# Kernel optimization log

Hardware: AMD Instinct MI355X
Metric: run time of the kernel (lower is better)

Reference implementation:

```python
import jax, jax.numpy as jnp
import numpy as np

V, D, H, DH, DI, L = 10000, 512, 8, 64, 2048, 12
B, S = 4, 1024
MAX_KLEN = 1024 + 0 + 512  # tgt_len + ext_len + mem_len
EPS = 1e-5
STD = 0.02


def setup_inputs() -> dict:
    key = jax.random.key(0)
    ks = jax.random.split(key, 10)
    data = jax.random.randint(ks[0], (B, S), 0, V)
    word_emb = jax.random.normal(ks[1], (V, D), jnp.float32) * STD
    pos_emb = jax.random.normal(ks[2], (MAX_KLEN, D), jnp.float32) * STD
    Wq = jax.random.normal(ks[3], (L, H * DH, D), jnp.float32) * STD
    Wkv = jax.random.normal(ks[4], (L, 2 * H * DH, D), jnp.float32) * STD
    Wo = jax.random.normal(ks[5], (L, D, H * DH), jnp.float32) * STD
    ln1_g = jnp.ones((L, D), jnp.float32)
    ln1_b = jnp.zeros((L, D), jnp.float32)
    W1 = jax.random.normal(ks[6], (L, DI, D), jnp.float32) * STD
    b1 = jnp.zeros((L, DI), jnp.float32)
    W2 = jax.random.normal(ks[7], (L, D, DI), jnp.float32) * STD
    b2 = jnp.zeros((L, D), jnp.float32)
    ln2_g = jnp.ones((L, D), jnp.float32)
    ln2_b = jnp.zeros((L, D), jnp.float32)
    out_b = jnp.zeros((V,), jnp.float32)  # out_layer weight is tied to word_emb
    return dict(data=data, word_emb=word_emb, pos_emb=pos_emb, Wq=Wq, Wkv=Wkv,
                Wo=Wo, ln1_g=ln1_g, ln1_b=ln1_b, W1=W1, b1=b1, W2=W2, b2=b2,
                ln2_g=ln2_g, ln2_b=ln2_b, out_b=out_b)


def _layernorm(x, g, b):
    m = jnp.mean(x, axis=-1, keepdims=True)
    v = jnp.mean((x - m) ** 2, axis=-1, keepdims=True)
    return (x - m) * jax.lax.rsqrt(v + EPS) * g + b


def reference(data, word_emb, pos_emb, Wq, Wkv, Wo, ln1_g, ln1_b,
              W1, b1, W2, b2, ln2_g, ln2_b, out_b):
    # mems start empty -> mlen = 0, klen = qlen, standard causal mask.
    h = word_emb[data] + pos_emb[:S][None, :, :]      # [B, S, D]
    mask = jnp.triu(jnp.ones((S, S), bool), 1)        # True above diagonal
    scale = 1.0 / np.sqrt(DH)

    def layer(h, p):
        wq, wkv, wo, g1, bl1, w1, bf1, w2, bf2, g2, bl2 = p
        q = (h @ wq.T).reshape(B, S, H, DH)
        k, v = jnp.split(h @ wkv.T, 2, axis=-1)
        k = k.reshape(B, S, H, DH)
        v = v.reshape(B, S, H, DH)
        sc = jnp.einsum('bqhd,bkhd->bhqk', q, k) * scale
        sc = jnp.where(mask[None, None], -jnp.inf, sc)
        p_attn = jax.nn.softmax(sc, axis=-1)           # [B, H, S, S] materialized
        av = jnp.einsum('bhqk,bkhd->bqhd', p_attn, v).reshape(B, S, H * DH)
        h = _layernorm(h + av @ wo.T, g1, bl1)         # post-LN (pre_lnorm=False)
        ff = jax.nn.relu(h @ w1.T + bf1) @ w2.T + bf2
        h = _layernorm(h + ff, g2, bl2)
        return h, None

    h, _ = jax.lax.scan(layer, h,
                        (Wq, Wkv, Wo, ln1_g, ln1_b, W1, b1, W2, b2, ln2_g, ln2_b))
    logits = h @ word_emb.T + out_b                    # tied output projection
    return logits                                      # [B, S, V]
```

## Files before the change

### kernel.cpp

```cpp
#include <hip/hip_runtime.h>

#define VV 10000
#define DD 512
#define HH 8
#define DH 64
#define DI 2048
#define LL 12
#define BB 4
#define SS 1024
#define TT (BB * SS)


typedef __attribute__((ext_vector_type(8))) short bhalf8;
typedef __attribute__((ext_vector_type(16))) float f32x16;

__device__ __forceinline__ void split_bf16(float x, unsigned short& h, unsigned short& l)
{
    unsigned int u = __float_as_uint(x);
    unsigned int r = (u + 0x7FFFu + ((u >> 16) & 1u)) & 0xFFFF0000u;
    h = (unsigned short)(r >> 16);
    float lf = x - __uint_as_float(r);
    unsigned int ul = __float_as_uint(lf);
    l = (unsigned short)((ul + 0x7FFFu + ((ul >> 16) & 1u)) >> 16);
}

__global__ __launch_bounds__(256) void convsplit(
    const float* __restrict__ src, unsigned short* __restrict__ hi,
    unsigned short* __restrict__ lo, int n4)
{
    int stride = gridDim.x * 256;
    for (int i = blockIdx.x * 256 + threadIdx.x; i < n4; i += stride) {
        float4 v = ((const float4*)src)[i];
        ushort4 h, l;
        split_bf16(v.x, h.x, l.x);
        split_bf16(v.y, h.y, l.y);
        split_bf16(v.z, h.z, l.z);
        split_bf16(v.w, h.w, l.w);
        ((ushort4*)hi)[i] = h;
        ((ushort4*)lo)[i] = l;
    }
}

__global__ __launch_bounds__(256) void embed_kernel(
    const int* __restrict__ data, const float* __restrict__ we,
    const float* __restrict__ pe, float* __restrict__ h,
    unsigned short* __restrict__ hhi, unsigned short* __restrict__ hlo)
{
    int tok = blockIdx.x;
    int tid = threadIdx.x;
    int idx = data[tok];
    int s = tok & (SS - 1);
    size_t base = (size_t)tok * DD;
    size_t wb = (size_t)idx * DD;
    size_t pb = (size_t)s * DD;
    float a = we[wb + tid] + pe[pb + tid];
    float b = we[wb + 256 + tid] + pe[pb + 256 + tid];
    h[base + tid] = a;
    h[base + 256 + tid] = b;
    unsigned short hx, lx;
    split_bf16(a, hx, lx); hhi[base + tid] = hx;       hlo[base + tid] = lx;
    split_bf16(b, hx, lx); hhi[base + 256 + tid] = hx; hlo[base + 256 + tid] = lx;
}

template<int BN, int EPI, bool SWZ>
__global__ __launch_bounds__(256) void gemm_mfma(
    const unsigned short* __restrict__ Ahp, const unsigned short* __restrict__ Alp,
    const unsigned short* __restrict__ Whp, const unsigned short* __restrict__ Wlp,
    const float* __restrict__ bias, float* __restrict__ C,
    unsigned short* __restrict__ Chp, unsigned short* __restrict__ Clp,
    unsigned short* __restrict__ Vhp, unsigned short* __restrict__ Vlp,
    int N, int K)
{
    constexpr int FN  = BN / 64;
    constexpr int BT  = BN * 128;
    constexpr int NBG = BN / 8;
    constexpr int NGRP = 32 + 2 * NBG;
    constexpr int PW  = NGRP / 4;
    __shared__ __align__(16) char smem[32768 + 2 * BT];

    int bx = blockIdx.x, by = blockIdx.y;
    if (SWZ) {
        int nwg = gridDim.x * gridDim.y;
        int id = by * gridDim.x + bx;
        int nq = nwg >> 3, rr = nwg & 7;
        int xcd = id & 7, j = id >> 3;
        int nid = (xcd < rr) ? (xcd * (nq + 1) + j)
                             : (rr * (nq + 1) + (xcd - rr) * nq + j);
        bx = nid % gridDim.x;
        by = nid / gridDim.x;
    }

    const int tid   = threadIdx.x;
    const int lane  = tid & 63;
    const int wid   = tid >> 6;
    const int wm    = wid >> 1;
    const int wn    = wid & 1;
    const int laneM = lane & 31;
    const int laneK = lane >> 5;
    const int m0    = by * 128;
    const int n0    = bx * BN;
    const int srow8 = lane >> 3;
    const int sslot = lane & 7;

    f32x16 acc[2][FN];
    #pragma unroll
    for (int i = 0; i < 2; ++i)
        #pragma unroll
        for (int j = 0; j < FN; ++j)
            #pragma unroll
            for (int r = 0; r < 16; ++r) acc[i][j][r] = 0.f;

    for (int k0 = 0; k0 < K; k0 += 64) {
        __syncthreads();
        bhalf8 rbuf[PW];
        #pragma unroll
        for (int t = 0; t < PW; ++t) {
            int g = wid * PW + t;
            const unsigned short* src;
            if (g < 32) {
                const unsigned short* bp = (g < 16) ? Ahp : Alp;
                int row = (g & 15) * 8 + srow8;
                src = bp + (size_t)(m0 + row) * K + (k0 + sslot * 8);
            } else {
                int d = g - 32;
                const unsigned short* bp = (d < NBG) ? Whp : Wlp;
                int row = (d & (NBG - 1)) * 8 + srow8;
                int n = n0 + row;
                n = (n < N) ? n : (N - 1);
                src = bp + (size_t)n * K + (k0 + sslot * 8);
            }
            rbuf[t] = *(const bhalf8*)src;
        }
        #pragma unroll
        for (int t = 0; t < PW; ++t) {
            int g = wid * PW + t;
            int off;
            if (g < 32) {
                int row = (g & 15) * 8 + srow8;
                off = ((g >> 4) << 14) + sslot * 2048 + ((row ^ sslot) << 4);
            } else {
                int d = g - 32;
                int row = (d & (NBG - 1)) * 8 + srow8;
                off = 32768 + ((d < NBG) ? 0 : BT)
                    + sslot * (BN * 16) + ((row ^ sslot) << 4);
            }
            *(bhalf8*)(smem + off) = rbuf[t];
        }
        __syncthreads();

        #pragma unroll
        for (int kb = 0; kb < 4; ++kb) {
            const int slot = kb * 2 + laneK;
            bhalf8 ah[2], al[2], bh[FN], bl[FN];
            #pragma unroll
            for (int i = 0; i < 2; ++i) {
                int row = wm * 64 + i * 32 + laneM;
                int off = slot * 2048 + ((row ^ slot) << 4);
                ah[i] = *(const bhalf8*)(smem + off);
                al[i] = *(const bhalf8*)(smem + 16384 + off);
            }
            #pragma unroll
            for (int j = 0; j < FN; ++j) {
                int row = wn * (BN / 2) + j * 32 + laneM;
                int off = 32768 + slot * (BN * 16) + ((row ^ slot) << 4);
                bh[j] = *(const bhalf8*)(smem + off);
                bl[j] = *(const bhalf8*)(smem + BT + off);
            }
            #pragma unroll
            for (int i = 0; i < 2; ++i)
                #pragma unroll
                for (int j = 0; j < FN; ++j) {
                    acc[i][j] = __builtin_amdgcn_mfma_f32_32x32x16_bf16(ah[i], bh[j], acc[i][j], 0, 0, 0);
                    acc[i][j] = __builtin_amdgcn_mfma_f32_32x32x16_bf16(ah[i], bl[j], acc[i][j], 0, 0, 0);
                    acc[i][j] = __builtin_amdgcn_mfma_f32_32x32x16_bf16(al[i], bh[j], acc[i][j], 0, 0, 0);
                }
        }
    }

    #pragma unroll
    for (int j = 0; j < FN; ++j) {
        int ncol = n0 + wn * (BN / 2) + j * 32 + laneM;
        bool nok = (ncol < N);
        float bv = 0.f;
        if (EPI == 1 || EPI == 2) { if (nok) bv = bias[ncol]; }
        #pragma unroll
        for (int i = 0; i < 2; ++i) {
            #pragma unroll
            for (int r = 0; r < 16; ++r) {
                int mrow = m0 + wm * 64 + i * 32 + (r & 3) + ((r >> 2) << 3) + laneK * 4;
                float v = acc[i][j][r] + bv;
                if (EPI == 2) v = fmaxf(v, 0.f);
                if (nok) {
                    if (EPI == 2 || EPI == 3) {
                        unsigned short hx, lx;
                        split_bf16(v, hx, lx);
                        Chp[(size_t)mrow * N + ncol] = hx;
                        Clp[(size_t)mrow * N + ncol] = lx;
                    } else if (EPI == 4) {
                        unsigned short hx, lx;
                        split_bf16(v, hx, lx);
                        if (ncol < 512) {
                            Chp[(size_t)mrow * 512 + ncol] = hx;
                            Clp[(size_t)mrow * 512 + ncol] = lx;
                        } else {
                            Vhp[(size_t)(ncol - 512) * TT + mrow] = hx;
                            Vlp[(size_t)(ncol - 512) * TT + mrow] = lx;
                        }
                    } else {
                        C[(size_t)mrow * N + ncol] = v;
                    }
                }
            }
        }
    }
}

__global__ __launch_bounds__(128) void flash_mfma(
    const unsigned short* __restrict__ qhp, const unsigned short* __restrict__ qlp,
    const unsigned short* __restrict__ khp, const unsigned short* __restrict__ klp,
    const unsigned short* __restrict__ vthp, const unsigned short* __restrict__ vtlp,
    unsigned short* __restrict__ avh, unsigned short* __restrict__ avl)
{
    __shared__ __align__(16) char lds[50176];

    const int qt  = 15 - (int)blockIdx.x;
    const int hh  = blockIdx.y;
    const int b   = blockIdx.z;
    const int tid = threadIdx.x;
    const int lane  = tid & 63;
    const int wq    = tid >> 6;
    const int laneM = lane & 31;
    const int laneK = lane >> 5;
    const int q0    = qt * 64;

    bhalf8 Qh[4], Ql[4];
    {
        size_t qoff = (size_t)(b * SS + q0 + 32 * wq + laneM) * 512 + hh * 64 + 8 * laneK;
        #pragma unroll
        for (int ks = 0; ks < 4; ++ks) {
            Qh[ks] = *(const bhalf8*)(qhp + qoff + 16 * ks);
            Ql[ks] = *(const bhalf8*)(qlp + qoff + 16 * ks);
        }
    }

    f32x16 O0, O1;
    #pragma unroll
    for (int r = 0; r < 16; ++r) { O0[r] = 0.f; O1[r] = 0.f; }
    float mrun = -1e30f, lrun = 0.f;

    const int srow  = tid >> 1;
    const int shalf = tid & 1;
    float* Pl = (float*)(lds + 32768 + wq * 8704);

    for (int kt = 0; kt <= qt; ++kt) {
        __syncthreads();
        {
            size_t kbase = (size_t)(b * SS + kt * 64 + srow) * 512 + hh * 64 + 32 * shalf;
            size_t vbase = (size_t)(hh * 64 + srow) * TT + b * SS + kt * 64 + 32 * shalf;
            bhalf8 k0[4], k1[4], v0[4], v1[4];
            #pragma unroll
            for (int j = 0; j < 4; ++j) {
                k0[j] = *(const bhalf8*)(khp  + kbase + 8 * j);
                k1[j] = *(const bhalf8*)(klp  + kbase + 8 * j);
                v0[j] = *(const bhalf8*)(vthp + vbase + 8 * j);
                v1[j] = *(const bhalf8*)(vtlp + vbase + 8 * j);
            }
            int ob = srow * 128 + 64 * shalf;
            int sw = (srow & 7) << 4;
            #pragma unroll
            for (int j = 0; j < 4; ++j) {
                int o = (ob + 16 * j) ^ sw;
                *(bhalf8*)(lds + o)         = k0[j];
                *(bhalf8*)(lds + 8192 + o)  = k1[j];
                *(bhalf8*)(lds + 16384 + o) = v0[j];
                *(bhalf8*)(lds + 24576 + o) = v1[j];
            }
        }
        __syncthreads();

        f32x16 s0, s1;
        #pragma unroll
        for (int r = 0; r < 16; ++r) { s0[r] = 0.f; s1[r] = 0.f; }
        #pragma unroll
        for (int ks = 0; ks < 4; ++ks) {
            int db = 32 * ks + 16 * laneK;
            int o0 = (laneM * 128 + db) ^ ((laneM & 7) << 4);
            int r1 = 32 + laneM;
            int o1 = (r1 * 128 + db) ^ ((r1 & 7) << 4);
            bhalf8 kh0 = *(const bhalf8*)(lds + o0);
            bhalf8 kl0 = *(const bhalf8*)(lds + 8192 + o0);
            bhalf8 kh1 = *(const bhalf8*)(lds + o1);
            bhalf8 kl1 = *(const bhalf8*)(lds + 8192 + o1);
            s0 = __builtin_amdgcn_mfma_f32_32x32x16_bf16(kh0, Qh[ks], s0, 0, 0, 0);
            s0 = __builtin_amdgcn_mfma_f32_32x32x16_bf16(kh0, Ql[ks], s0, 0, 0, 0);
            s0 = __builtin_amdgcn_mfma_f32_32x32x16_bf16(kl0, Qh[ks], s0, 0, 0, 0);
            s1 = __builtin_amdgcn_mfma_f32_32x32x16_bf16(kh1, Qh[ks], s1, 0, 0, 0);
            s1 = __builtin_amdgcn_mfma_f32_32x32x16_bf16(kh1, Ql[ks], s1, 0, 0, 0);
            s1 = __builtin_amdgcn_mfma_f32_32x32x16_bf16(kl1, Qh[ks], s1, 0, 0, 0);
        }

        #pragma unroll
        for (int r = 0; r < 16; ++r) { s0[r] *= 0.125f; s1[r] *= 0.125f; }

        if (kt == qt) {
            int qrel = 32 * wq + laneM;
            #pragma unroll
            for (int r = 0; r < 16; ++r) {
                int krel = (r & 3) + ((r >> 2) << 3) + 4 * laneK;
                if (krel > qrel)      s0[r] = -1e30f;
                if (krel + 32 > qrel) s1[r] = -1e30f;
            }
        }

        float mx = s0[0];
        #pragma unroll
        for (int r = 1; r < 16; ++r) mx = fmaxf(mx, s0[r]);
        #pragma unroll
        for (int r = 0; r < 16; ++r) mx = fmaxf(mx, s1[r]);
        mx = fmaxf(mx, __shfl_xor(mx, 32));
        float mn = fmaxf(mrun, mx);
        float alpha = __expf(mrun - mn);
        mrun = mn;
        float rs = 0.f;
        #pragma unroll
        for (int r = 0; r < 16; ++r) {
            float p0 = __expf(s0[r] - mn);
            float p1 = __expf(s1[r] - mn);
            s0[r] = p0; s1[r] = p1;
            rs += p0 + p1;
        }
        rs += __shfl_xor(rs, 32);
        lrun = lrun * alpha + rs;
        #pragma unroll
        for (int r = 0; r < 16; ++r) { O0[r] *= alpha; O1[r] *= alpha; }

        #pragma unroll
        for (int r = 0; r < 16; ++r) {
            int krel = (r & 3) + ((r >> 2) << 3) + 4 * laneK;
            Pl[laneM * 68 + krel]      = s0[r];
            Pl[laneM * 68 + 32 + krel] = s1[r];
        }
        __asm__ volatile("s_waitcnt lgkmcnt(0)" ::: "memory");
        __builtin_amdgcn_sched_barrier(0);

        #pragma unroll
        for (int ks = 0; ks < 4; ++ks) {
            const float* pr = &Pl[laneM * 68 + 16 * ks + 8 * laneK];
            float4 pa = *(const float4*)pr;
            float4 pb = *(const float4*)(pr + 4);
            float pv[8] = {pa.x, pa.y, pa.z, pa.w, pb.x, pb.y, pb.z, pb.w};
            bhalf8 ph, plo;
            #pragma unroll
            for (int i = 0; i < 8; ++i) {
                unsigned u = __float_as_uint(pv[i]);
                ph[i] = (short)(u >> 16);
                float lf = pv[i] - __uint_as_float(u & 0xFFFF0000u);
                plo[i] = (short)(__float_as_uint(lf) >> 16);
            }
            int db = 32 * ks + 16 * laneK;
            {
                int col = laneM;
                int o = (col * 128 + db) ^ ((col & 7) << 4);
                bhalf8 vh = *(const bhalf8*)(lds + 16384 + o);
                bhalf8 vl = *(const bhalf8*)(lds + 24576 + o);
                O0 = __builtin_amdgcn_mfma_f32_32x32x16_bf16(vh, ph,  O0, 0, 0, 0);
                O0 = __builtin_amdgcn_mfma_f32_32x32x16_bf16(vl, ph,  O0, 0, 0, 0);
                O0 = __builtin_amdgcn_mfma_f32_32x32x16_bf16(vh, plo, O0, 0, 0, 0);
            }
            {
                int col = 32 + laneM;
                int o = (col * 128 + db) ^ ((col & 7) << 4);
                bhalf8 vh = *(const bhalf8*)(lds + 16384 + o);
                bhalf8 vl = *(const bhalf8*)(lds + 24576 + o);
                O1 = __builtin_amdgcn_mfma_f32_32x32x16_bf16(vh, ph,  O1, 0, 0, 0);
                O1 = __builtin_amdgcn_mfma_f32_32x32x16_bf16(vl, ph,  O1, 0, 0, 0);
                O1 = __builtin_amdgcn_mfma_f32_32x32x16_bf16(vh, plo, O1, 0, 0, 0);
            }
        }
    }

    float inv = 1.0f / lrun;
    #pragma unroll
    for (int r = 0; r < 16; ++r) {
        int d = (r & 3) + ((r >> 2) << 3) + 4 * laneK;
        Pl[laneM * 68 + d]      = O0[r] * inv;
        Pl[laneM * 68 + 32 + d] = O1[r] * inv;
    }
    __asm__ volatile("s_waitcnt lgkmcnt(0)" ::: "memory");
    __builtin_amdgcn_sched_barrier(0);
    #pragma unroll
    for (int it = 0; it < 16; ++it) {
        int qr = it * 2 + (lane >> 5);
        int d  = (lane & 31) * 2;
        float2 v = *(const float2*)&Pl[qr * 68 + d];
        unsigned short h0, l0, h1, l1;
        split_bf16(v.x, h0, l0);
        split_bf16(v.y, h1, l1);
        size_t base = (size_t)(b * SS + q0 + 32 * wq + qr) * 512 + hh * 64 + d;
        ushort2 hv; hv.x = h0; hv.y = h1;
        ushort2 lv; lv.x = l0; lv.y = l1;
        *(ushort2*)(avh + base) = hv;
        *(ushort2*)(avl + base) = lv;
    }
}

__global__ __launch_bounds__(256) void add_ln_kernel(
    float* __restrict__ h, const float* __restrict__ x,
    const float* __restrict__ g, const float* __restrict__ bta,
    unsigned short* __restrict__ hhi, unsigned short* __restrict__ hlo)
{
    int tok = blockIdx.x, tid = threadIdx.x;
    size_t base = (size_t)tok * DD;
    float v0 = h[base + tid] + x[base + tid];
    float v1 = h[base + 256 + tid] + x[base + 256 + tid];

    __shared__ float rs[256], rq[256];
    rs[tid] = v0 + v1;
    rq[tid] = v0 * v0 + v1 * v1;
    __syncthreads();
    for (int off = 128; off > 0; off >>= 1) {
        if (tid < off) { rs[tid] += rs[tid + off]; rq[tid] += rq[tid + off]; }
        __syncthreads();
    }
    float mean = rs[0] * (1.f / 512.f);
    float var  = rq[0] * (1.f / 512.f) - mean * mean;
    float inv  = rsqrtf(var + 1e-5f);
    float o0 = (v0 - mean) * inv * g[tid]       + bta[tid];
    float o1 = (v1 - mean) * inv * g[256 + tid] + bta[256 + tid];
    h[base + tid]       = o0;
    h[base + 256 + tid] = o1;
    unsigned short a, b;
    split_bf16(o0, a, b); hhi[base + tid]       = a; hlo[base + tid]       = b;
    split_bf16(o1, a, b); hhi[base + 256 + tid] = a; hlo[base + 256 + tid] = b;
}

extern "C" void kernel_launch(void* const* d_in, const int* in_sizes, int n_in,
                              void* d_out, int out_size, void* d_ws, size_t ws_size,
                              hipStream_t stream)
{
    const int*   data = (const int*)d_in[0];
    const float* we   = (const float*)d_in[1];
    const float* pe   = (const float*)d_in[2];
    const float* Wq   = (const float*)d_in[3];
    const float* Wkv  = (const float*)d_in[4];
    const float* Wo   = (const float*)d_in[5];
    const float* g1   = (const float*)d_in[6];
    const float* bl1  = (const float*)d_in[7];
    const float* W1   = (const float*)d_in[8];
    const float* b1   = (const float*)d_in[9];
    const float* W2   = (const float*)d_in[10];
    const float* b2   = (const float*)d_in[11];
    const float* g2   = (const float*)d_in[12];
    const float* bl2  = (const float*)d_in[13];
    const float* outb = (const float*)d_in[14];
    float* out = (float*)d_out;

    typedef unsigned short us;
    float* h    = (float*)d_ws;
    us* qhp  = (us*)(h + (size_t)TT * 512);
    us* qlp  = qhp  + (size_t)TT * 512;
    us* khp  = qlp  + (size_t)TT * 512;
    us* klp  = khp  + (size_t)TT * 512;
    us* vthp = klp  + (size_t)TT * 512;
    us* vtlp = vthp + (size_t)TT * 512;
    us* avh  = vtlp + (size_t)TT * 512;
    us* avl  = avh  + (size_t)TT * 512;
    float* tmp = (float*)(avl + (size_t)TT * 512);
    us* hhi  = (us*)(tmp + (size_t)TT * 512);
    us* hlo  = hhi + (size_t)TT * 512;
    us* ffh = qhp;
    us* ffl = qhp + (size_t)TT * 2048;
    us* wqh  = hlo + (size_t)TT * 512;
    us* wql  = wqh  + (size_t)LL * 512 * 512;
    us* wkvh = wql  + (size_t)LL * 512 * 512;
    us* wkvl = wkvh + (size_t)LL * 1024 * 512;
    us* woh  = wkvl + (size_t)LL * 1024 * 512;
    us* wol  = woh  + (size_t)LL * 512 * 512;
    us* w1h  = wol  + (size_t)LL * 512 * 512;
    us* w1l  = w1h  + (size_t)LL * 2048 * 512;
    us* w2h  = w1l  + (size_t)LL * 2048 * 512;
    us* w2l  = w2h  + (size_t)LL * 512 * 2048;
    us* weh  = w2l  + (size_t)LL * 512 * 2048;
    us* wel  = weh  + (size_t)VV * 512;

    auto cv = [&](const float* s, us* hh, us* ll, size_t n) {
        int n4 = (int)(n >> 2);
        int blocks = (n4 + 255) / 256;
        if (blocks > 2048) blocks = 2048;
        convsplit<<<blocks, 256, 0, stream>>>(s, hh, ll, n4);
    };
    cv(Wq,  wqh,  wql,  (size_t)LL * 512 * 512);
    cv(Wkv, wkvh, wkvl, (size_t)LL * 1024 * 512);
    cv(Wo,  woh,  wol,  (size_t)LL * 512 * 512);
    cv(W1,  w1h,  w1l,  (size_t)LL * 2048 * 512);
    cv(W2,  w2h,  w2l,  (size_t)LL * 512 * 2048);
    cv(we,  weh,  wel,  (size_t)VV * 512);

    embed_kernel<<<TT, 256, 0, stream>>>(data, we, pe, h, hhi, hlo);

    for (int l = 0; l < LL; ++l) {
        const us* lwqh  = wqh  + (size_t)l * 512 * 512;
        const us* lwql  = wql  + (size_t)l * 512 * 512;
        const us* lwkvh = wkvh + (size_t)l * 1024 * 512;
        const us* lwkvl = wkvl + (size_t)l * 1024 * 512;
        const us* lwoh  = woh  + (size_t)l * 512 * 512;
        const us* lwol  = wol  + (size_t)l * 512 * 512;
        const us* lw1h  = w1h  + (size_t)l * 2048 * 512;
        const us* lw1l  = w1l  + (size_t)l * 2048 * 512;
        const us* lw2h  = w2h  + (size_t)l * 512 * 2048;
        const us* lw2l  = w2l  + (size_t)l * 512 * 2048;

        gemm_mfma<64, 3, false><<<dim3(8, 32), 256, 0, stream>>>(
            hhi, hlo, lwqh, lwql, nullptr, nullptr, qhp, qlp, nullptr, nullptr, 512, 512);
        gemm_mfma<128, 4, false><<<dim3(8, 32), 256, 0, stream>>>(
            hhi, hlo, lwkvh, lwkvl, nullptr, nullptr, khp, klp, vthp, vtlp, 1024, 512);
        flash_mfma<<<dim3(16, HH, BB), 128, 0, stream>>>(
            qhp, qlp, khp, klp, vthp, vtlp, avh, avl);
        gemm_mfma<64, 0, false><<<dim3(8, 32), 256, 0, stream>>>(
            avh, avl, lwoh, lwol, nullptr, tmp, nullptr, nullptr, nullptr, nullptr, 512, 512);
        add_ln_kernel<<<TT, 256, 0, stream>>>(h, tmp, g1 + l * 512, bl1 + l * 512, hhi, hlo);
        gemm_mfma<128, 2, false><<<dim3(16, 32), 256, 0, stream>>>(
            hhi, hlo, lw1h, lw1l, b1 + l * 2048, nullptr, ffh, ffl, nullptr, nullptr, 2048, 512);
        gemm_mfma<64, 1, false><<<dim3(8, 32), 256, 0, stream>>>(
            ffh, ffl, lw2h, lw2l, b2 + l * 512, tmp, nullptr, nullptr, nullptr, nullptr, 512, 2048);
        add_ln_kernel<<<TT, 256, 0, stream>>>(h, tmp, g2 + l * 512, bl2 + l * 512, hhi, hlo);
    }

    gemm_mfma<128, 1, true><<<dim3((VV + 127) / 128, 32), 256, 0, stream>>>(
        hhi, hlo, weh, wel, outb, out, nullptr, nullptr, nullptr, nullptr, VV, 512);
}
```

Baseline: 3.500 ms.

## Use direct global-to-LDS loads in GEMM and attention, add MFMA priority hints

Replaces the register-staged global-load-then-LDS-store tile fills in both the GEMM and the flash-attention kernels with global_load_lds (16-byte) transfers. The XOR swizzle moves into the per-lane source addresses, because the LDS destination is now contiguous per wave. In attention, one wave pair loads K and the other loads V, and s_setprio is raised around the MFMA blocks. The XCD swizzle is also hardcoded to a fixed 79-wide grid with a 10-column grouping, which ties that path to one problem shape. The aim is lower VGPR pressure and less load/store instruction overhead. The risk is wrong results if the swizzle math or the grid assumption is off for other launches.

```diff
diff --git a/kernel.cpp b/kernel.cpp
--- a/kernel.cpp
+++ b/kernel.cpp
@@ -13,6 +13,13 @@
 
 typedef __attribute__((ext_vector_type(8))) short bhalf8;
 typedef __attribute__((ext_vector_type(16))) float f32x16;
+
+__device__ __forceinline__ void gload16(const unsigned short* g, void* l)
+{
+    __builtin_amdgcn_global_load_lds(
+        (const __attribute__((address_space(1))) void*)g,
+        (__attribute__((address_space(3))) void*)l, 16, 0, 0);
+}
 
 __device__ __forceinline__ void split_bf16(float x, unsigned short& h, unsigned short& l)
 {
@@ -73,21 +80,17 @@
 {
     constexpr int FN  = BN / 64;
     constexpr int BT  = BN * 128;
-    constexpr int NBG = BN / 8;
-    constexpr int NGRP = 32 + 2 * NBG;
-    constexpr int PW  = NGRP / 4;
+    constexpr int NWB = BN / 8;
+    constexpr int NW  = 32 + 2 * NWB;
+    constexpr int WPW = NW / 4;
     __shared__ __align__(16) char smem[32768 + 2 * BT];
 
     int bx = blockIdx.x, by = blockIdx.y;
     if (SWZ) {
-        int nwg = gridDim.x * gridDim.y;
-        int id = by * gridDim.x + bx;
-        int nq = nwg >> 3, rr = nwg & 7;
-        int xcd = id & 7, j = id >> 3;
-        int nid = (xcd < rr) ? (xcd * (nq + 1) + j)
-                             : (rr * (nq + 1) + (xcd - rr) * nq + j);
-        bx = nid % gridDim.x;
-        by = nid / gridDim.x;
+        int id = by * 79 + bx;
+        int t  = (id & 7) * 316 + (id >> 3);
+        if (t < 2240) { int c = t / 320, r = t - c * 320; by = r / 10; bx = c * 10 + r % 10; }
+        else          { int r = t - 2240;                 by = r / 9;  bx = 70 + r % 9; }
     }
 
     const int tid   = threadIdx.x;
@@ -99,8 +102,29 @@
     const int laneK = lane >> 5;
     const int m0    = by * 128;
     const int n0    = bx * BN;
-    const int srow8 = lane >> 3;
-    const int sslot = lane & 7;
+
+    const unsigned short* wsrc[WPW];
+    #pragma unroll
+    for (int t = 0; t < WPW; ++t) {
+        int w = wid * WPW + t;
+        if (w < 32) {
+            const unsigned short* bp = (w < 16) ? Ahp : Alp;
+            int wa = w & 15;
+            int slot = wa >> 1;
+            int row = (((wa & 1) << 6) | lane) ^ slot;
+            wsrc[t] = bp + (size_t)(m0 + row) * K + slot * 8;
+        } else {
+            int d = w - 32;
+            const unsigned short* bp = (d < NWB) ? Whp : Wlp;
+            int wb = d & (NWB - 1);
+            int slot, row;
+            if (BN == 64) { slot = wb;      row = lane ^ slot; }
+            else          { slot = wb >> 1; row = (((wb & 1) << 6) | lane) ^ slot; }
+            int n = n0 + row;
+            n = (n < N) ? n : (N - 1);
+            wsrc[t] = bp + (size_t)n * K + slot * 8;
+        }
+    }
 
     f32x16 acc[2][FN];
     #pragma unroll
@@ -112,40 +136,9 @@
 
     for (int k0 = 0; k0 < K; k0 += 64) {
         __syncthreads();
-        bhalf8 rbuf[PW];
-        #pragma unroll
-        for (int t = 0; t < PW; ++t) {
-            int g = wid * PW + t;
-            const unsigned short* src;
-            if (g < 32) {
-                const unsigned short* bp = (g < 16) ? Ahp : Alp;
-                int row = (g & 15) * 8 + srow8;
-                src = bp + (size_t)(m0 + row) * K + (k0 + sslot * 8);
-            } else {
-                int d = g - 32;
-                const unsigned short* bp = (d < NBG) ? Whp : Wlp;
-                int row = (d & (NBG - 1)) * 8 + srow8;
-                int n = n0 + row;
-                n = (n < N) ? n : (N - 1);
-                src = bp + (size_t)n * K + (k0 + sslot * 8);
-            }
-            rbuf[t] = *(const bhalf8*)src;
-        }
-        #pragma unroll
-        for (int t = 0; t < PW; ++t) {
-            int g = wid * PW + t;
-            int off;
-            if (g < 32) {
-                int row = (g & 15) * 8 + srow8;
-                off = ((g >> 4) << 14) + sslot * 2048 + ((row ^ sslot) << 4);
-            } else {
-                int d = g - 32;
-                int row = (d & (NBG - 1)) * 8 + srow8;
-                off = 32768 + ((d < NBG) ? 0 : BT)
-                    + sslot * (BN * 16) + ((row ^ sslot) << 4);
-            }
-            *(bhalf8*)(smem + off) = rbuf[t];
-        }
+        #pragma unroll
+        for (int t = 0; t < WPW; ++t)
+            gload16(wsrc[t] + k0, smem + (wid * WPW + t) * 1024);
         __syncthreads();
 
         #pragma unroll
@@ -248,39 +241,29 @@
     for (int r = 0; r < 16; ++r) { O0[r] = 0.f; O1[r] = 0.f; }
     float mrun = -1e30f, lrun = 0.f;
 
-    const int srow  = tid >> 1;
-    const int shalf = tid & 1;
     float* Pl = (float*)(lds + 32768 + wq * 8704);
+    const unsigned short* shi = wq ? vthp : khp;
+    const unsigned short* slo = wq ? vtlp : klp;
+    char* dbase = lds + wq * 16384;
 
     for (int kt = 0; kt <= qt; ++kt) {
         __syncthreads();
-        {
-            size_t kbase = (size_t)(b * SS + kt * 64 + srow) * 512 + hh * 64 + 32 * shalf;
-            size_t vbase = (size_t)(hh * 64 + srow) * TT + b * SS + kt * 64 + 32 * shalf;
-            bhalf8 k0[4], k1[4], v0[4], v1[4];
-            #pragma unroll
-            for (int j = 0; j < 4; ++j) {
-                k0[j] = *(const bhalf8*)(khp  + kbase + 8 * j);
-                k1[j] = *(const bhalf8*)(klp  + kbase + 8 * j);
-                v0[j] = *(const bhalf8*)(vthp + vbase + 8 * j);
-                v1[j] = *(const bhalf8*)(vtlp + vbase + 8 * j);
-            }
-            int ob = srow * 128 + 64 * shalf;
-            int sw = (srow & 7) << 4;
-            #pragma unroll
-            for (int j = 0; j < 4; ++j) {
-                int o = (ob + 16 * j) ^ sw;
-                *(bhalf8*)(lds + o)         = k0[j];
-                *(bhalf8*)(lds + 8192 + o)  = k1[j];
-                *(bhalf8*)(lds + 16384 + o) = v0[j];
-                *(bhalf8*)(lds + 24576 + o) = v1[j];
-            }
+        #pragma unroll
+        for (int t = 0; t < 8; ++t) {
+            int o   = t * 1024 + lane * 16;
+            int row = o >> 7;
+            int eo  = ((o & 127) ^ ((row & 7) << 4)) >> 1;
+            size_t rb = wq ? ((size_t)(hh * 64 + row) * TT + (size_t)b * SS + kt * 64)
+                           : ((size_t)(b * SS + kt * 64 + row) * 512 + hh * 64);
+            gload16(shi + rb + eo, dbase + t * 1024);
+            gload16(slo + rb + eo, dbase + 8192 + t * 1024);
         }
         __syncthreads();
 
         f32x16 s0, s1;
         #pragma unroll
         for (int r = 0; r < 16; ++r) { s0[r] = 0.f; s1[r] = 0.f; }
+        __builtin_amdgcn_s_setprio(1);
         #pragma unroll
         for (int ks = 0; ks < 4; ++ks) {
             int db = 32 * ks + 16 * laneK;
@@ -298,6 +281,7 @@
             s1 = __builtin_amdgcn_mfma_f32_32x32x16_bf16(kh1, Ql[ks], s1, 0, 0, 0);
             s1 = __builtin_amdgcn_mfma_f32_32x32x16_bf16(kl1, Qh[ks], s1, 0, 0, 0);
         }
+        __builtin_amdgcn_s_setprio(0);
 
         #pragma unroll
         for (int r = 0; r < 16; ++r) { s0[r] *= 0.125f; s1[r] *= 0.125f; }
@@ -358,6 +342,7 @@
                 plo[i] = (short)(__float_as_uint(lf) >> 16);
             }
             int db = 32 * ks + 16 * laneK;
+            __builtin_amdgcn_s_setprio(1);
             {
                 int col = laneM;
                 int o = (col * 128 + db) ^ ((col & 7) << 4);
@@ -376,6 +361,7 @@
                 O1 = __builtin_amdgcn_mfma_f32_32x32x16_bf16(vl, ph,  O1, 0, 0, 0);
                 O1 = __builtin_amdgcn_mfma_f32_32x32x16_bf16(vh, plo, O1, 0, 0, 0);
             }
+            __builtin_amdgcn_s_setprio(0);
         }
     }
 
```

Result: slower. 5.089 ms (+45.4%).
